# Kernel optimization log

Hardware: AMD Instinct MI355X
Metric: run time of the kernel (lower is better)

## Reference

```python
import jax, jax.numpy as jnp
import numpy as np

B, L, C, H = 2, 4096, 512, 8
DH = C // H


def setup_inputs() -> dict:
    key = jax.random.key(0)
    ks = jax.random.split(key, 6)
    s = 1.0 / np.sqrt(C)
    return {
        "x": jax.random.normal(ks[0], (B, L, C), dtype=jnp.float32),
        "Wq": jax.random.normal(ks[1], (C, C), dtype=jnp.float32) * s,
        "Wk": jax.random.normal(ks[2], (C, C), dtype=jnp.float32) * s,
        "Wv": jax.random.normal(ks[3], (C, C), dtype=jnp.float32) * s,
        "Wo": jax.random.normal(ks[4], (C, C), dtype=jnp.float32) * s,
        "bo": jnp.zeros((C,), dtype=jnp.float32),
    }


def reference(x, Wq, Wk, Wv, Wo, bo):
    # x: [B, L, C]; split heads -> [B, H, L, Dh]
    def heads(t):
        return t.reshape(B, L, H, DH).transpose(0, 2, 1, 3)

    q = heads(x @ Wq)
    k = heads(x @ Wk)
    v = heads(x @ Wv)
    scale = 1.0 / np.sqrt(DH)
    scores = jnp.einsum("bhqd,bhkd->bhqk", q, k) * scale  # [B,H,L,L]
    w = jax.nn.softmax(scores, axis=-1)  # dropout_rate=0.0 -> identity
    att = jnp.einsum("bhqk,bhkd->bhqd", w, v)  # [B,H,L,Dh]
    att = att.transpose(0, 2, 1, 3).reshape(B, L, C)
    return att @ Wo + bo
```

## Files before the change

### kernel.cpp

```cpp
#include <hip/hip_runtime.h>
#include <hip/hip_bf16.h>

typedef __hip_bfloat16 bh;
typedef __attribute__((ext_vector_type(8))) __bf16 bf16x8;
typedef __attribute__((ext_vector_type(4))) float f32x4;
typedef __attribute__((ext_vector_type(4))) int i32x4;
typedef __attribute__((ext_vector_type(4))) short s16x4;

#define NB 2
#define NL 4096
#define NC 512
#define NH 8
#define NDH 64
#define NM (NB * NL)
#define LOG2E 1.4426950408889634f
#define KVBLK 8192

static __device__ __forceinline__ f32x4 mfma_bf16(bf16x8 a, bf16x8 b, f32x4 c) {
    return __builtin_amdgcn_mfma_f32_16x16x32_bf16(a, b, c, 0, 0, 0);
}
static __device__ __forceinline__ f32x4 mfma16(s16x4 a, s16x4 b, f32x4 c) {
    return __builtin_amdgcn_mfma_f32_16x16x16bf16_1k(a, b, c, 0, 0, 0);
}

static __device__ __forceinline__ void st_bf4(bh* dst, float a, float b, float c, float d) {
    bh tmp[4] = {__float2bfloat16(a), __float2bfloat16(b),
                 __float2bfloat16(c), __float2bfloat16(d)};
    *(s16x4*)dst = *(const s16x4*)tmp;
}
static __device__ __forceinline__ s16x4 pk_bf4(float a, float b, float c, float d) {
    bh tmp[4] = {__float2bfloat16(a), __float2bfloat16(b),
                 __float2bfloat16(c), __float2bfloat16(d)};
    return *(const s16x4*)tmp;
}

static __device__ __forceinline__ void gload16(const bh* g, bh* l) {
    __builtin_amdgcn_global_load_lds(
        (const __attribute__((address_space(1))) void*)g,
        (__attribute__((address_space(3))) void*)l,
        16, 0, 0);
}

__global__ __launch_bounds__(256, 2)
void prep(const float* __restrict__ x,
          const float* __restrict__ Wq, const float* __restrict__ Wk,
          const float* __restrict__ Wv, const float* __restrict__ Wo,
          bh* __restrict__ xf, bh* __restrict__ Wf)
{
    const int t = threadIdx.x;
    const int wave = t >> 6, lane = t & 63;
    const int quad = lane >> 4, c16 = lane & 15;

    if (blockIdx.z < 8) {
        __shared__ __align__(16) bh T[64][72];
        const int m64 = blockIdx.x, k64 = blockIdx.z;
        #pragma unroll
        for (int rep = 0; rep < 4; rep++) {
            int li = t + rep * 256;
            int r = li >> 4, c4 = (li & 15) * 4;
            float4 f = *(const float4*)&x[(size_t)(m64 * 64 + r) * 512 + k64 * 64 + c4];
            st_bf4(&T[r][c4], f.x, f.y, f.z, f.w);
        }
        __syncthreads();
        #pragma unroll
        for (int kcl = 0; kcl < 2; kcl++) {
            i32x4 v = *(const i32x4*)&T[wave * 16 + c16][kcl * 32 + quad * 8];
            size_t addr = ((size_t)(m64 * 4 + wave) * 16 + (k64 * 2 + kcl)) * 512 + lane * 8;
            *(i32x4*)&xf[addr] = v;
        }
    } else {
        if (blockIdx.x >= 64) return;
        int task = blockIdx.x * 4 + wave;
        int z = task >> 6, nt = (task >> 3) & 7, k0i = task & 7;
        const float* W = (z == 0) ? Wq : (z == 1) ? Wk : (z == 2) ? Wv : Wo;
        bh* dst = Wf + (((size_t)z * 8 + nt) * 8 + k0i) * 4096;
        #pragma unroll
        for (int kc = 0; kc < 2; kc++)
            #pragma unroll
            for (int fn = 0; fn < 4; fn++) {
                bh tmp[8];
                #pragma unroll
                for (int j = 0; j < 8; j++)
                    tmp[j] = __float2bfloat16(
                        W[(size_t)(k0i * 64 + kc * 32 + quad * 8 + j) * 512
                          + nt * 64 + fn * 16 + c16]);
                *(i32x4*)&dst[(kc * 4 + fn) * 512 + lane * 8] = *(const i32x4*)tmp;
            }
    }
}

__global__ __launch_bounds__(256, 3)
void qkv_gemm(const bh* __restrict__ xf, const bh* __restrict__ Wf,
              bh* __restrict__ Qb, bh* __restrict__ KVf)
{
    __shared__ __align__(16) bh smem[8192 + 3 * 4096];
    bh* Xl = smem;
    bh* Wl = smem + 8192;

    const int t = threadIdx.x;
    const int wave = t >> 6, lane = t & 63;
    const int quad = lane >> 4, c16 = lane & 15;
    const int m0 = blockIdx.x * 128;
    const int nt = blockIdx.y;
    const int m16b = m0 >> 4;

    f32x4 acc[3][2][4];
    for (int z = 0; z < 3; z++)
        for (int a = 0; a < 2; a++)
            for (int b = 0; b < 4; b++)
                for (int u = 0; u < 4; u++) acc[z][a][b][u] = 0.0f;

    for (int k0i = 0; k0i < 8; k0i++) {
        #pragma unroll
        for (int r = 0; r < 4; r++) {
            int f = wave * 4 + r;
            const bh* src = xf + ((size_t)(m16b + (f >> 1)) * 16 + k0i * 2 + (f & 1)) * 512
                          + lane * 8;
            gload16(src, &Xl[f * 512 + lane * 8]);
        }
        #pragma unroll
        for (int z = 0; z < 3; z++) {
            const bh* wz = Wf + (((size_t)z * 8 + nt) * 8 + k0i) * 4096;
            #pragma unroll
            for (int r = 0; r < 2; r++) {
                int off = (wave * 2 + r) * 512 + lane * 8;
                gload16(wz + off, &Wl[z * 4096 + off]);
            }
        }
        __syncthreads();
        #pragma unroll
        for (int kc = 0; kc < 2; kc++) {
            bf16x8 af0 = *(const bf16x8*)&Xl[((wave * 2 + 0) * 2 + kc) * 512 + lane * 8];
            bf16x8 af1 = *(const bf16x8*)&Xl[((wave * 2 + 1) * 2 + kc) * 512 + lane * 8];
            #pragma unroll
            for (int z = 0; z < 3; z++)
                #pragma unroll
                for (int fn = 0; fn < 4; fn++) {
                    bf16x8 bf = *(const bf16x8*)&Wl[z * 4096 + (kc * 4 + fn) * 512 + lane * 8];
                    acc[z][0][fn] = mfma_bf16(af0, bf, acc[z][0][fn]);
                    acc[z][1][fn] = mfma_bf16(af1, bf, acc[z][1][fn]);
                }
        }
        __syncthreads();
    }

    const int h = nt;
    const int b = m0 >> 12;
    const int l0 = m0 & 4095;
    const int bh_i = b * NH + h;
    const int kt0 = l0 >> 6;

    {
        bh* Tq = smem;
        #pragma unroll
        for (int fm = 0; fm < 2; fm++)
            #pragma unroll
            for (int i = 0; i < 4; i++) {
                int ll = wave * 32 + fm * 16 + quad * 4 + i;
                #pragma unroll
                for (int fn = 0; fn < 4; fn++)
                    Tq[ll * 68 + fn * 16 + c16] =
                        __float2bfloat16(acc[0][fm][fn][i] * 0.125f);
            }
        __syncthreads();
        int l = t >> 1, half = t & 1;
        bh* dst = Qb + ((size_t)bh_i * NL + l0 + l) * NDH + half * 32;
        const bh* src = &Tq[l * 68 + half * 32];
        #pragma unroll
        for (int r = 0; r < 4; r++)
            *(i32x4*)(dst + r * 8) = *(const i32x4*)(src + r * 8);
        __syncthreads();
    }

    {
        bh* Tk = smem;
        #pragma unroll
        for (int fm = 0; fm < 2; fm++)
            #pragma unroll
            for (int i = 0; i < 4; i++) {
                int ll = wave * 32 + fm * 16 + quad * 4 + i;
                int ktl = ll >> 6, l64 = ll & 63;
                int fk = l64 >> 4, c16t = l64 & 15;
                #pragma unroll
                for (int fn = 0; fn < 4; fn++) {
                    int d = fn * 16 + c16;
                    int kc = d >> 5, qt = (d >> 3) & 3, j = d & 7;
                    Tk[ktl * 4096 + (fk * 2 + kc) * 512 + (qt * 16 + c16t) * 8 + j] =
                        __float2bfloat16(acc[1][fm][fn][i] * LOG2E);
                }
            }
        __syncthreads();
        int idx = t * 32;
        int ktl = idx >> 12, wi = idx & 4095;
        bh* dst = KVf + (size_t)(bh_i * 64 + kt0 + ktl) * KVBLK + wi;
        #pragma unroll
        for (int r = 0; r < 4; r++)
            *(i32x4*)(dst + r * 8) = *(const i32x4*)&Tk[idx + r * 8];
    }

    #pragma unroll
    for (int fm = 0; fm < 2; fm++) {
        int fkv = (wave * 2 + fm) & 3;
        int ktv = kt0 + (wave >> 1);
        #pragma unroll
        for (int fn = 0; fn < 4; fn++) {
            size_t addr = (size_t)(bh_i * 64 + ktv) * KVBLK + 4096
                        + (size_t)(fn * 4 + fkv) * 256 + (quad * 16 + c16) * 4;
            st_bf4(&KVf[addr], acc[2][fm][fn][0], acc[2][fm][fn][1],
                               acc[2][fm][fn][2], acc[2][fm][fn][3]);
        }
    }
}

__global__ __launch_bounds__(512, 4)
void flash_attn(const bh* __restrict__ Qb, const bh* __restrict__ KVf,
                bh* __restrict__ attb)
{
    __shared__ __align__(16) bh SF[2][2][KVBLK];

    const int t = threadIdx.x;
    const int wave = t >> 6, lane = t & 63;
    const int group = wave >> 2, w4 = wave & 3;
    const int quad = lane >> 4, c16 = lane & 15;
    const int bh_idx = blockIdx.y;
    const int q0 = blockIdx.x * 128;

    const bh* Qp  = Qb + (size_t)bh_idx * NL * NDH;
    const bh* KVp = KVf + (size_t)bh_idx * 64 * KVBLK;

    bf16x8 qf[2][2];
    #pragma unroll
    for (int fq = 0; fq < 2; fq++)
        #pragma unroll
        for (int kc = 0; kc < 2; kc++)
            qf[fq][kc] = *(const bf16x8*)
                &Qp[(size_t)(q0 + w4 * 32 + fq * 16 + c16) * NDH + kc * 32 + quad * 8];

    f32x4 ot[4][2];
    float lsum[2] = {0.0f, 0.0f};
    for (int a = 0; a < 4; a++)
        for (int fq = 0; fq < 2; fq++)
            for (int u = 0; u < 4; u++) ot[a][fq][u] = 0.0f;

    auto stage = [&](int i, int buf) {
        int kt = 2 * i + group;
        #pragma unroll
        for (int r = 0; r < 4; r++) {
            int off = (w4 * 4 + r) * 512 + lane * 8;
            gload16(KVp + (size_t)kt * KVBLK + off, &SF[group][buf][off]);
        }
    };

    stage(0, 0);
    for (int i = 0; i < 32; i++) {
        const int buf = i & 1;
        __syncthreads();
        if (i < 31) stage(i + 1, buf ^ 1);
        const bh* sf = &SF[group][buf][0];

        f32x4 s[4][2];
        for (int a = 0; a < 4; a++)
            for (int fq = 0; fq < 2; fq++)
                for (int u = 0; u < 4; u++) s[a][fq][u] = 0.0f;
        #pragma unroll
        for (int kc = 0; kc < 2; kc++)
            #pragma unroll
            for (int fk = 0; fk < 4; fk++) {
                bf16x8 kf = *(const bf16x8*)&sf[(fk * 2 + kc) * 512 + lane * 8];
                s[fk][0] = mfma_bf16(kf, qf[0][kc], s[fk][0]);
                s[fk][1] = mfma_bf16(kf, qf[1][kc], s[fk][1]);
            }

        s16x4 vt[4][4];
        #pragma unroll
        for (int fn = 0; fn < 4; fn++)
            #pragma unroll
            for (int fk = 0; fk < 4; fk++)
                vt[fn][fk] = *(const s16x4*)&sf[4096 + (fn * 4 + fk) * 256 + lane * 4];

        s16x4 pf[4][2];
        float rs0 = 0.0f, rs1 = 0.0f;
        #pragma unroll
        for (int fk = 0; fk < 4; fk++) {
            float a0 = __builtin_amdgcn_exp2f(s[fk][0][0]);
            float a1 = __builtin_amdgcn_exp2f(s[fk][0][1]);
            float a2 = __builtin_amdgcn_exp2f(s[fk][0][2]);
            float a3 = __builtin_amdgcn_exp2f(s[fk][0][3]);
            rs0 += (a0 + a1) + (a2 + a3);
            pf[fk][0] = pk_bf4(a0, a1, a2, a3);
            float b0 = __builtin_amdgcn_exp2f(s[fk][1][0]);
            float b1 = __builtin_amdgcn_exp2f(s[fk][1][1]);
            float b2 = __builtin_amdgcn_exp2f(s[fk][1][2]);
            float b3 = __builtin_amdgcn_exp2f(s[fk][1][3]);
            rs1 += (b0 + b1) + (b2 + b3);
            pf[fk][1] = pk_bf4(b0, b1, b2, b3);
        }
        lsum[0] += rs0;
        lsum[1] += rs1;

        #pragma unroll
        for (int fk = 0; fk < 4; fk++)
            #pragma unroll
            for (int fn = 0; fn < 4; fn++) {
                ot[fn][0] = mfma16(vt[fn][fk], pf[fk][0], ot[fn][0]);
                ot[fn][1] = mfma16(vt[fn][fk], pf[fk][1], ot[fn][1]);
            }
    }

    #pragma unroll
    for (int fq = 0; fq < 2; fq++) {
        lsum[fq] += __shfl_xor(lsum[fq], 16);
        lsum[fq] += __shfl_xor(lsum[fq], 32);
    }

    float* Ocmb = (float*)&SF[0][0][0];
    float* Lcmb = Ocmb + 128 * 64;
    __syncthreads();
    if (group == 1) {
        #pragma unroll
        for (int fq = 0; fq < 2; fq++) {
            int q = w4 * 32 + fq * 16 + c16;
            #pragma unroll
            for (int fn = 0; fn < 4; fn++)
                *(f32x4*)&Ocmb[q * 64 + fn * 16 + quad * 4] = ot[fn][fq];
            if (quad == 0) Lcmb[q] = lsum[fq];
        }
    }
    __syncthreads();
    if (group == 0) {
        const int b = bh_idx >> 3, h = bh_idx & 7;
        #pragma unroll
        for (int fq = 0; fq < 2; fq++) {
            int q = w4 * 32 + fq * 16 + c16;
            float inv = 1.0f / (lsum[fq] + Lcmb[q]);
            size_t rowbase = ((size_t)b * NL + (q0 + q)) * NC + h * NDH;
            #pragma unroll
            for (int fn = 0; fn < 4; fn++) {
                f32x4 o2 = *(const f32x4*)&Ocmb[q * 64 + fn * 16 + quad * 4];
                st_bf4(&attb[rowbase + fn * 16 + quad * 4],
                       (ot[fn][fq][0] + o2[0]) * inv, (ot[fn][fq][1] + o2[1]) * inv,
                       (ot[fn][fq][2] + o2[2]) * inv, (ot[fn][fq][3] + o2[3]) * inv);
            }
        }
    }
}

__global__ __launch_bounds__(256, 4)
void out_gemm(const bh* __restrict__ A, const bh* __restrict__ Wf,
              const float* __restrict__ bo, float* __restrict__ out)
{
    __shared__ __align__(16) bh Xs[128][72];
    __shared__ __align__(16) bh Wl[4096];

    const int t = threadIdx.x;
    const int wave = t >> 6, lane = t & 63;
    const int quad = lane >> 4, c16 = lane & 15;
    const int m0 = blockIdx.x * 128;
    const int nt = blockIdx.y;
    const int n0 = nt * 64;

    f32x4 acc[2][4];
    for (int a = 0; a < 2; a++)
        for (int b = 0; b < 4; b++)
            for (int u = 0; u < 4; u++) acc[a][b][u] = 0.0f;

    for (int k0i = 0; k0i < 8; k0i++) {
        const bh* wz = Wf + (((size_t)3 * 8 + nt) * 8 + k0i) * 4096;
        #pragma unroll
        for (int r = 0; r < 2; r++) {
            int off = (wave * 2 + r) * 512 + lane * 8;
            gload16(wz + off, &Wl[off]);
        }
        #pragma unroll
        for (int rep = 0; rep < 4; rep++) {
            int li = t + rep * 256;
            int r = li >> 3, d0 = (li & 7) * 8;
            *(i32x4*)&Xs[r][d0] = *(const i32x4*)&A[(size_t)(m0 + r) * 512 + k0i * 64 + d0];
        }
        __syncthreads();
        #pragma unroll
        for (int kc = 0; kc < 2; kc++) {
            bf16x8 af0 = *(const bf16x8*)&Xs[wave * 32 +      c16][kc * 32 + quad * 8];
            bf16x8 af1 = *(const bf16x8*)&Xs[wave * 32 + 16 + c16][kc * 32 + quad * 8];
            #pragma unroll
            for (int fn = 0; fn < 4; fn++) {
                bf16x8 bf = *(const bf16x8*)&Wl[(kc * 4 + fn) * 512 + lane * 8];
                acc[0][fn] = mfma_bf16(af0, bf, acc[0][fn]);
                acc[1][fn] = mfma_bf16(af1, bf, acc[1][fn]);
            }
        }
        __syncthreads();
    }

    #pragma unroll
    for (int fm = 0; fm < 2; fm++)
        #pragma unroll
        for (int i = 0; i < 4; i++) {
            int mr = m0 + wave * 32 + fm * 16 + quad * 4 + i;
            #pragma unroll
            for (int fn = 0; fn < 4; fn++) {
                int cn = n0 + fn * 16 + c16;
                out[(size_t)mr * 512 + cn] = acc[fm][fn][i] + bo[cn];
            }
        }
}

extern "C" void kernel_launch(void* const* d_in, const int* in_sizes, int n_in,
                              void* d_out, int out_size, void* d_ws, size_t ws_size,
                              hipStream_t stream)
{
    const float* x  = (const float*)d_in[0];
    const float* Wq = (const float*)d_in[1];
    const float* Wk = (const float*)d_in[2];
    const float* Wv = (const float*)d_in[3];
    const float* Wo = (const float*)d_in[4];
    const float* bo = (const float*)d_in[5];
    float* out = (float*)d_out;

    const size_t mat = (size_t)NM * NC;
    bh* Qb   = (bh*)d_ws;
    bh* KVf  = Qb + mat;
    bh* attb = KVf + 2 * mat;
    bh* Wf   = attb + mat;
    bh* xf   = Wf + 4 * 8 * 8 * 4096;

    prep      <<<dim3(128, 1, 9),         256, 0, stream>>>(x, Wq, Wk, Wv, Wo, xf, Wf);
    qkv_gemm  <<<dim3(NM / 128, NC / 64), 256, 0, stream>>>(xf, Wf, Qb, KVf);
    flash_attn<<<dim3(NL / 128, NB * NH), 512, 0, stream>>>(Qb, KVf, attb);
    out_gemm  <<<dim3(NM / 128, NC / 64), 256, 0, stream>>>(attb, Wf, bo, out);
}
```

Before: 190.5 us.

## Double-buffer GEMM tiles and emit attention output in fragment layout

The QKV and output projection GEMMs now use double-buffered shared memory, so the next K-slice is loaded while the current one is multiplied. The attention kernel writes its output in the pre-swizzled fragment layout the QKV input uses, which lets out_gemm stream A with direct global-to-LDS loads instead of row-major copies. The score MFMA chain starts from a zero constant instead of zero-initialised accumulators. In exchange, shared memory per block doubles and the launch bounds drop to 2 blocks per SM, which lowers occupancy.

```diff
diff --git a/kernel.cpp b/kernel.cpp
--- a/kernel.cpp
+++ b/kernel.cpp
@@ -89,13 +89,11 @@
     }
 }
 
-__global__ __launch_bounds__(256, 3)
+__global__ __launch_bounds__(256, 2)
 void qkv_gemm(const bh* __restrict__ xf, const bh* __restrict__ Wf,
               bh* __restrict__ Qb, bh* __restrict__ KVf)
 {
-    __shared__ __align__(16) bh smem[8192 + 3 * 4096];
-    bh* Xl = smem;
-    bh* Wl = smem + 8192;
+    __shared__ __align__(16) bh smem[2][20480];
 
     const int t = threadIdx.x;
     const int wave = t >> 6, lane = t & 63;
@@ -110,7 +108,9 @@
             for (int b = 0; b < 4; b++)
                 for (int u = 0; u < 4; u++) acc[z][a][b][u] = 0.0f;
 
-    for (int k0i = 0; k0i < 8; k0i++) {
+    auto stage = [&](int k0i, int buf) {
+        bh* Xl = &smem[buf][0];
+        bh* Wl = &smem[buf][8192];
         #pragma unroll
         for (int r = 0; r < 4; r++) {
             int f = wave * 4 + r;
@@ -127,7 +127,15 @@
                 gload16(wz + off, &Wl[z * 4096 + off]);
             }
         }
-        __syncthreads();
+    };
+
+    stage(0, 0);
+    for (int k0i = 0; k0i < 8; k0i++) {
+        const int buf = k0i & 1;
+        __syncthreads();
+        if (k0i < 7) stage(k0i + 1, buf ^ 1);
+        const bh* Xl = &smem[buf][0];
+        const bh* Wl = &smem[buf][8192];
         #pragma unroll
         for (int kc = 0; kc < 2; kc++) {
             bf16x8 af0 = *(const bf16x8*)&Xl[((wave * 2 + 0) * 2 + kc) * 512 + lane * 8];
@@ -151,7 +159,7 @@
     const int kt0 = l0 >> 6;
 
     {
-        bh* Tq = smem;
+        bh* Tq = &smem[0][0];
         #pragma unroll
         for (int fm = 0; fm < 2; fm++)
             #pragma unroll
@@ -173,7 +181,7 @@
     }
 
     {
-        bh* Tk = smem;
+        bh* Tk = &smem[0][0];
         #pragma unroll
         for (int fm = 0; fm < 2; fm++)
             #pragma unroll
@@ -241,6 +249,7 @@
     for (int a = 0; a < 4; a++)
         for (int fq = 0; fq < 2; fq++)
             for (int u = 0; u < 4; u++) ot[a][fq][u] = 0.0f;
+    const f32x4 z4 = {0.0f, 0.0f, 0.0f, 0.0f};
 
     auto stage = [&](int i, int buf) {
         int kt = 2 * i + group;
@@ -259,17 +268,18 @@
         const bh* sf = &SF[group][buf][0];
 
         f32x4 s[4][2];
-        for (int a = 0; a < 4; a++)
-            for (int fq = 0; fq < 2; fq++)
-                for (int u = 0; u < 4; u++) s[a][fq][u] = 0.0f;
-        #pragma unroll
-        for (int kc = 0; kc < 2; kc++)
-            #pragma unroll
-            for (int fk = 0; fk < 4; fk++) {
-                bf16x8 kf = *(const bf16x8*)&sf[(fk * 2 + kc) * 512 + lane * 8];
-                s[fk][0] = mfma_bf16(kf, qf[0][kc], s[fk][0]);
-                s[fk][1] = mfma_bf16(kf, qf[1][kc], s[fk][1]);
-            }
+        #pragma unroll
+        for (int fk = 0; fk < 4; fk++) {
+            bf16x8 kf0 = *(const bf16x8*)&sf[(fk * 2 + 0) * 512 + lane * 8];
+            s[fk][0] = mfma_bf16(kf0, qf[0][0], z4);
+            s[fk][1] = mfma_bf16(kf0, qf[1][0], z4);
+        }
+        #pragma unroll
+        for (int fk = 0; fk < 4; fk++) {
+            bf16x8 kf1 = *(const bf16x8*)&sf[(fk * 2 + 1) * 512 + lane * 8];
+            s[fk][0] = mfma_bf16(kf1, qf[0][1], s[fk][0]);
+            s[fk][1] = mfma_bf16(kf1, qf[1][1], s[fk][1]);
+        }
 
         s16x4 vt[4][4];
         #pragma unroll
@@ -329,15 +339,19 @@
     __syncthreads();
     if (group == 0) {
         const int b = bh_idx >> 3, h = bh_idx & 7;
+        const int mbase16 = (b * NL + q0) >> 4;
         #pragma unroll
         for (int fq = 0; fq < 2; fq++) {
             int q = w4 * 32 + fq * 16 + c16;
             float inv = 1.0f / (lsum[fq] + Lcmb[q]);
-            size_t rowbase = ((size_t)b * NL + (q0 + q)) * NC + h * NDH;
+            int m16 = mbase16 + w4 * 2 + fq;
             #pragma unroll
             for (int fn = 0; fn < 4; fn++) {
                 f32x4 o2 = *(const f32x4*)&Ocmb[q * 64 + fn * 16 + quad * 4];
-                st_bf4(&attb[rowbase + fn * 16 + quad * 4],
+                size_t addr = ((size_t)m16 * 16 + h * 2 + (fn >> 1)) * 512
+                            + (size_t)(((fn & 1) * 2 + (quad >> 1)) * 16 + c16) * 8
+                            + (quad & 1) * 4;
+                st_bf4(&attb[addr],
                        (ot[fn][fq][0] + o2[0]) * inv, (ot[fn][fq][1] + o2[1]) * inv,
                        (ot[fn][fq][2] + o2[2]) * inv, (ot[fn][fq][3] + o2[3]) * inv);
             }
@@ -345,12 +359,11 @@
     }
 }
 
-__global__ __launch_bounds__(256, 4)
-void out_gemm(const bh* __restrict__ A, const bh* __restrict__ Wf,
+__global__ __launch_bounds__(256, 2)
+void out_gemm(const bh* __restrict__ Af, const bh* __restrict__ Wf,
               const float* __restrict__ bo, float* __restrict__ out)
 {
-    __shared__ __align__(16) bh Xs[128][72];
-    __shared__ __align__(16) bh Wl[4096];
+    __shared__ __align__(16) bh smem[2][12288];
 
     const int t = threadIdx.x;
     const int wave = t >> 6, lane = t & 63;
@@ -358,30 +371,42 @@
     const int m0 = blockIdx.x * 128;
     const int nt = blockIdx.y;
     const int n0 = nt * 64;
+    const int m16b = m0 >> 4;
 
     f32x4 acc[2][4];
     for (int a = 0; a < 2; a++)
         for (int b = 0; b < 4; b++)
             for (int u = 0; u < 4; u++) acc[a][b][u] = 0.0f;
 
-    for (int k0i = 0; k0i < 8; k0i++) {
+    auto stage = [&](int k0i, int buf) {
+        bh* Xl = &smem[buf][0];
+        bh* Wl = &smem[buf][8192];
+        #pragma unroll
+        for (int r = 0; r < 4; r++) {
+            int f = wave * 4 + r;
+            const bh* src = Af + ((size_t)(m16b + (f >> 1)) * 16 + k0i * 2 + (f & 1)) * 512
+                          + lane * 8;
+            gload16(src, &Xl[f * 512 + lane * 8]);
+        }
         const bh* wz = Wf + (((size_t)3 * 8 + nt) * 8 + k0i) * 4096;
         #pragma unroll
         for (int r = 0; r < 2; r++) {
             int off = (wave * 2 + r) * 512 + lane * 8;
             gload16(wz + off, &Wl[off]);
         }
-        #pragma unroll
-        for (int rep = 0; rep < 4; rep++) {
-            int li = t + rep * 256;
-            int r = li >> 3, d0 = (li & 7) * 8;
-            *(i32x4*)&Xs[r][d0] = *(const i32x4*)&A[(size_t)(m0 + r) * 512 + k0i * 64 + d0];
-        }
-        __syncthreads();
+    };
+
+    stage(0, 0);
+    for (int k0i = 0; k0i < 8; k0i++) {
+        const int buf = k0i & 1;
+        __syncthreads();
+        if (k0i < 7) stage(k0i + 1, buf ^ 1);
+        const bh* Xl = &smem[buf][0];
+        const bh* Wl = &smem[buf][8192];
         #pragma unroll
         for (int kc = 0; kc < 2; kc++) {
-            bf16x8 af0 = *(const bf16x8*)&Xs[wave * 32 +      c16][kc * 32 + quad * 8];
-            bf16x8 af1 = *(const bf16x8*)&Xs[wave * 32 + 16 + c16][kc * 32 + quad * 8];
+            bf16x8 af0 = *(const bf16x8*)&Xl[((wave * 2 + 0) * 2 + kc) * 512 + lane * 8];
+            bf16x8 af1 = *(const bf16x8*)&Xl[((wave * 2 + 1) * 2 + kc) * 512 + lane * 8];
             #pragma unroll
             for (int fn = 0; fn < 4; fn++) {
                 bf16x8 bf = *(const bf16x8*)&Wl[(kc * 4 + fn) * 512 + lane * 8];
```

New measurement: 186.9 us. No clear change (-1.9%).
